# Optimization experiments

Hardware: AMD Instinct MI355X
Metric: run time of the kernel (lower is better)

The kernel has to match this reference:

```python
import jax, jax.numpy as jnp
import numpy as np

N_NODES = 50000
N_EDGES = 800000
IN_FEATS = 256
OUT_FEATS = 128


def setup_inputs() -> dict:
    key = jax.random.key(0)
    k1, k2, k3, k4 = jax.random.split(key, 4)
    feat = jax.random.normal(k1, (N_NODES, IN_FEATS), dtype=jnp.float32)
    # xavier uniform init for weight [in, out]
    limit = float(np.sqrt(6.0 / (IN_FEATS + OUT_FEATS)))
    weight = jax.random.uniform(k2, (IN_FEATS, OUT_FEATS), minval=-limit, maxval=limit, dtype=jnp.float32)
    bias = jnp.zeros((OUT_FEATS,), dtype=jnp.float32)
    src = jax.random.randint(k3, (N_EDGES,), 0, N_NODES, dtype=jnp.int32)
    dst = jax.random.randint(k4, (N_EDGES,), 0, N_NODES, dtype=jnp.int32)
    return {"feat": feat, "weight": weight, "bias": bias, "src": src, "dst": dst}


def reference(feat, weight, bias, src, dst):
    N = feat.shape[0]
    in_f, out_f = weight.shape
    # right normalization: 1 / out_degree(src node), clamped to >= 1
    deg = jax.ops.segment_sum(jnp.ones(src.shape[0], dtype=feat.dtype), src, num_segments=N)
    norm = (1.0 / jnp.maximum(deg, 1.0))[:, None]  # [N,1]
    if in_f > out_f:
        # transform first (cheaper messages), then normalize + aggregate
        h = jnp.matmul(feat, weight) * norm          # [N, out]
        rst = jax.ops.segment_sum(h[src], dst, num_segments=N)  # scatter-sum over edges
    else:
        h = feat * norm                               # [N, in]
        rst = jax.ops.segment_sum(h[src], dst, num_segments=N)
        rst = jnp.matmul(rst, weight)
    return rst + bias
```

## Files before the change

### kernel.cpp

```cpp
#include <hip/hip_runtime.h>

#define N_NODES 50000
#define N_EDGES 800000
#define IN_F 256
#define OUT_F 128

#define CHUNKS 128
#define EPC (N_EDGES / CHUNKS)
#define BINW (N_NODES / 4)
#define NWORDS (N_NODES / 4)
#define RGB 196
#define HIST_BLOCKS (2 * CHUNKS)
#define CPW (CHUNKS / 4)

#define GEMM_START HIST_BLOCKS
#define GEMMF_BLOCKS 196
#define SCAT_BLOCKS 782

typedef __attribute__((ext_vector_type(8))) short short8;
typedef __attribute__((ext_vector_type(4))) float float4_t;

__device__ __forceinline__ short f2bf(float f) {
  unsigned u = __builtin_bit_cast(unsigned, f);
  u = u + 0x7FFFu + ((u >> 16) & 1u);
  return (short)(u >> 16);
}

__device__ __forceinline__ float bflo(unsigned u) {
  return __builtin_bit_cast(float, u << 16);
}
__device__ __forceinline__ float bfhi(unsigned u) {
  return __builtin_bit_cast(float, u & 0xFFFF0000u);
}

__global__ __launch_bounds__(512) void fused1_kernel(const int* __restrict__ src,
                                                     const int* __restrict__ dst,
                                                     unsigned char* __restrict__ pdst8,
                                                     unsigned char* __restrict__ psrc8,
                                                     unsigned char* __restrict__ rank8,
                                                     const float* __restrict__ W,
                                                     const float* __restrict__ feat,
                                                     unsigned short* __restrict__ h,
                                                     int* __restrict__ cursor) {
  __shared__ uint4 smem4[4096];
  int b = blockIdx.x;
  int tid = threadIdx.x;

  if (b >= GEMM_START) {
    if (b == GEMM_START && tid == 0) *cursor = 0;
    short* wl = (short*)smem4;
#pragma unroll
    for (int i = 0; i < 64; ++i) {
      int idx = i * 512 + tid;
      int k = idx >> 7, n = idx & 127;
      int s = k >> 5, q = (k >> 3) & 3, j = k & 7;
      int tt = n >> 4, m = n & 15;
      wl[((s * 8 + tt) * 64 + q * 16 + m) * 8 + j] = f2bf(W[idx]);
    }
    __syncthreads();

    int w = tid >> 6, l = tid & 63;
    int m = l & 15, q = l >> 4;
    long base = (long)(b - GEMM_START) * 256 + w * 32;

    float4_t acc[2][8];
#pragma unroll
    for (int r = 0; r < 2; ++r)
#pragma unroll
      for (int to = 0; to < 8; ++to) acc[r][to] = (float4_t)(0.0f);

    long row0 = base + m;
    long row1 = base + 16 + m;
    long r0c = row0 < N_NODES - 1 ? row0 : N_NODES - 1;
    long r1c = row1 < N_NODES - 1 ? row1 : N_NODES - 1;
    const float* a0p = feat + (size_t)r0c * IN_F;
    const float* a1p = feat + (size_t)r1c * IN_F;
    const short8* wl8 = (const short8*)smem4;

#pragma unroll
    for (int s = 0; s < 8; ++s) {
      int k0 = s * 32 + q * 8;
      float4_t av0a = *(const float4_t*)(a0p + k0);
      float4_t av0b = *(const float4_t*)(a0p + k0 + 4);
      float4_t av1a = *(const float4_t*)(a1p + k0);
      float4_t av1b = *(const float4_t*)(a1p + k0 + 4);
      short8 fa0, fa1;
#pragma unroll
      for (int i = 0; i < 4; ++i) {
        fa0[i] = f2bf(av0a[i]);
        fa0[i + 4] = f2bf(av0b[i]);
        fa1[i] = f2bf(av1a[i]);
        fa1[i + 4] = f2bf(av1b[i]);
      }
#pragma unroll
      for (int to = 0; to < 8; ++to) {
        short8 fb = wl8[(s * 8 + to) * 64 + l];
        acc[0][to] = __builtin_amdgcn_mfma_f32_16x16x32_bf16(fa0, fb, acc[0][to], 0, 0, 0);
        acc[1][to] = __builtin_amdgcn_mfma_f32_16x16x32_bf16(fa1, fb, acc[1][to], 0, 0, 0);
      }
    }

#pragma unroll
    for (int r = 0; r < 2; ++r) {
#pragma unroll
      for (int i = 0; i < 4; ++i) {
        long row = base + r * 16 + q * 4 + i;
        if (row < N_NODES) {
          size_t ho = (size_t)row * OUT_F;
#pragma unroll
          for (int to = 0; to < 8; ++to) {
            h[ho + to * 16 + m] = (unsigned short)f2bf(acc[r][to][i]);
          }
        }
      }
    }
    return;
  }

  unsigned* bins = (unsigned*)smem4;
  int hs = b >> 7;
  int c = b & 127;
  uint4* b4 = (uint4*)bins;
  for (int j = tid; j < BINW / 4; j += 512) b4[j] = (uint4){0u, 0u, 0u, 0u};
  __syncthreads();
  const int* key = hs ? src : dst;
  int e0 = c * EPC;

  auto process = [&](int v, int eI) {
    unsigned sh = (v & 3) * 8;
    unsigned old = atomicAdd(&bins[v >> 2], 1u << sh);
    if (!hs) rank8[eI] = (unsigned char)((old >> sh) & 0xFFu);
  };

#pragma unroll 2
  for (int tile = 0; tile < 3; ++tile) {
    int i = tile * 2048 + tid;
    int k0 = key[e0 + i];
    int k1 = key[e0 + i + 512];
    int k2 = key[e0 + i + 1024];
    int k3 = key[e0 + i + 1536];
    process(k0, e0 + i);
    process(k1, e0 + i + 512);
    process(k2, e0 + i + 1024);
    process(k3, e0 + i + 1536);
  }
  {
    int i = 6144 + tid;
    if (i < EPC) process(key[e0 + i], e0 + i);
  }
  __syncthreads();
  uint4* p128 = (uint4*)((hs ? psrc8 : pdst8) + (size_t)c * N_NODES);
  const uint4* s128 = (const uint4*)bins;
  for (int j = tid; j < BINW / 4; j += 512) p128[j] = s128[j];
}

__global__ __launch_bounds__(256) void reduceoff_kernel(const unsigned char* __restrict__ pdst8,
                                                        const unsigned char* __restrict__ psrc8,
                                                        unsigned char* __restrict__ delta8,
                                                        int* __restrict__ cnt,
                                                        int* __restrict__ row_start,
                                                        int* __restrict__ cursor,
                                                        float* __restrict__ norm) {
  __shared__ unsigned tot[4][64];
  int g = blockIdx.x, side = blockIdx.y;
  int t = threadIdx.x;
  int w = t >> 6, l = t & 63;
  int wd = g * 64 + l;
  bool ok = wd < NWORDS;
  int wdc = ok ? wd : NWORDS - 1;
  const unsigned* P = (const unsigned*)(side == 0 ? pdst8 : psrc8);

  unsigned vals[CPW];
  unsigned s = 0;
#pragma unroll
  for (int i = 0; i < CPW; ++i) {
    vals[i] = P[(size_t)(w * CPW + i) * NWORDS + wdc];
    s += vals[i];
  }
  tot[w][l] = s;
  __syncthreads();

  if (side == 0) {
    unsigned base = 0;
#pragma unroll
    for (int w2 = 0; w2 < 4; ++w2)
      if (w2 < w) base += tot[w2][l];
    unsigned run = base;
    unsigned* D = (unsigned*)delta8;
    if (ok) {
#pragma unroll
      for (int i = 0; i < CPW; ++i) {
        D[(size_t)(w * CPW + i) * NWORDS + wd] = run;
        run += vals[i];
      }
    }
    if (w == 0) {
      unsigned ftot = tot[0][l] + tot[1][l] + tot[2][l] + tot[3][l];
      if (!ok) ftot = 0;
      int c0 = ftot & 255, c1 = (ftot >> 8) & 255, c2 = (ftot >> 16) & 255, c3 = ftot >> 24;
      int T = c0 + c1 + c2 + c3;
      int x = T;
#pragma unroll
      for (int off = 1; off < 64; off <<= 1) {
        int y = __shfl_up(x, off);
        if (l >= off) x += y;
      }
      int waveTotal = __shfl(x, 63);
      int sb = 0;
      if (l == 63) sb = atomicAdd(cursor, waveTotal);
      sb = __shfl(sb, 63);
      int E = sb + x - T;
      if (ok) {
        int4 cv = {c0, c1, c2, c3};
        int4 rv = {E, E + c0, E + c0 + c1, E + c0 + c1 + c2};
        ((int4*)cnt)[wd] = cv;
        ((int4*)row_start)[wd] = rv;
      }
    }
  } else {
    if (w == 0 && ok) {
      unsigned ftot = tot[0][l] + tot[1][l] + tot[2][l] + tot[3][l];
      float4 nv;
      int d0 = ftot & 255, d1 = (ftot >> 8) & 255, d2 = (ftot >> 16) & 255, d3 = (int)(ftot >> 24);
      nv.x = 1.0f / (float)(d0 > 1 ? d0 : 1);
      nv.y = 1.0f / (float)(d1 > 1 ? d1 : 1);
      nv.z = 1.0f / (float)(d2 > 1 ? d2 : 1);
      nv.w = 1.0f / (float)(d3 > 1 ? d3 : 1);
      ((float4*)norm)[wd] = nv;
    }
  }
}

__global__ __launch_bounds__(256) void scat_kernel(const int* __restrict__ src,
                                                   const int* __restrict__ dst,
                                                   const int* __restrict__ row_start,
                                                   const unsigned char* __restrict__ delta8,
                                                   const unsigned char* __restrict__ rank8,
                                                   int* __restrict__ eidx) {
  int gt = blockIdx.x * 256 + threadIdx.x;
  int e = gt * 4;
  if (e >= N_EDGES) return;
  int4 d4 = *(const int4*)(dst + e);
  int4 s4 = *(const int4*)(src + e);
  unsigned rr = *(const unsigned*)(rank8 + e);
  int dd[4] = {d4.x, d4.y, d4.z, d4.w};
  int ss[4] = {s4.x, s4.y, s4.z, s4.w};
#pragma unroll
  for (int k = 0; k < 4; ++k) {
    int c = (e + k) / EPC;
    int d = dd[k];
    int pos = row_start[d] + (int)delta8[(size_t)c * N_NODES + d] + (int)((rr >> (8 * k)) & 0xFFu);
    eidx[pos] = ss[k];
  }
}

__global__ __launch_bounds__(256) void agg_kernel(const unsigned short* __restrict__ h,
                                                  const int* __restrict__ row_start,
                                                  const int* __restrict__ cnt,
                                                  const int* __restrict__ eidx,
                                                  const float* __restrict__ norm,
                                                  const float* __restrict__ bias,
                                                  float* __restrict__ out) {
  int w = threadIdx.x >> 6, l = threadIdx.x & 63;
  int d = blockIdx.x * 4 + w;
  int rs = row_start[d], re = rs + cnt[d];
  const uint4* __restrict__ hu4 = (const uint4*)h;
  int rowsel = l >> 4;
  int cp = l & 15;
  float a0 = 0.f, a1 = 0.f, a2 = 0.f, a3 = 0.f, a4 = 0.f, a5 = 0.f, a6 = 0.f, a7 = 0.f;

  auto acc8 = [&](uint4 v, float nm) {
    a0 = fmaf(bflo(v.x), nm, a0); a1 = fmaf(bfhi(v.x), nm, a1);
    a2 = fmaf(bflo(v.y), nm, a2); a3 = fmaf(bfhi(v.y), nm, a3);
    a4 = fmaf(bflo(v.z), nm, a4); a5 = fmaf(bfhi(v.z), nm, a5);
    a6 = fmaf(bflo(v.w), nm, a6); a7 = fmaf(bfhi(v.w), nm, a7);
  };

  for (int bse = rs; bse < re; bse += 64) {
    int n = re - bse; if (n > 64) n = 64;
    int e = (l < n) ? eidx[bse + l] : 0;
    int quarter = (n + 3) >> 2;
    int j = 0;
    for (; j + 4 <= quarter; j += 4) {
      int i0 = 4 * j + rowsel;
      int s0 = __shfl(e, i0);
      int s1 = __shfl(e, i0 + 4);
      int s2 = __shfl(e, i0 + 8);
      int s3 = __shfl(e, i0 + 12);
      uint4 v0 = hu4[(size_t)s0 * 16 + cp];
      uint4 v1 = hu4[(size_t)s1 * 16 + cp];
      uint4 v2 = hu4[(size_t)s2 * 16 + cp];
      uint4 v3 = hu4[(size_t)s3 * 16 + cp];
      float nm0 = norm[s0], nm1 = norm[s1], nm2 = norm[s2], nm3 = norm[s3];
      if (i0 >= n) v0 = (uint4){0u, 0u, 0u, 0u};
      if (i0 + 4 >= n) v1 = (uint4){0u, 0u, 0u, 0u};
      if (i0 + 8 >= n) v2 = (uint4){0u, 0u, 0u, 0u};
      if (i0 + 12 >= n) v3 = (uint4){0u, 0u, 0u, 0u};
      acc8(v0, nm0);
      acc8(v1, nm1);
      acc8(v2, nm2);
      acc8(v3, nm3);
    }
    for (; j < quarter; ++j) {
      int i0 = 4 * j + rowsel;
      int s0 = __shfl(e, i0);
      uint4 v0 = hu4[(size_t)s0 * 16 + cp];
      float nm0 = norm[s0];
      if (i0 >= n) v0 = (uint4){0u, 0u, 0u, 0u};
      acc8(v0, nm0);
    }
  }
  a0 += __shfl_xor(a0, 16); a1 += __shfl_xor(a1, 16);
  a2 += __shfl_xor(a2, 16); a3 += __shfl_xor(a3, 16);
  a4 += __shfl_xor(a4, 16); a5 += __shfl_xor(a5, 16);
  a6 += __shfl_xor(a6, 16); a7 += __shfl_xor(a7, 16);
  a0 += __shfl_xor(a0, 32); a1 += __shfl_xor(a1, 32);
  a2 += __shfl_xor(a2, 32); a3 += __shfl_xor(a3, 32);
  a4 += __shfl_xor(a4, 32); a5 += __shfl_xor(a5, 32);
  a6 += __shfl_xor(a6, 32); a7 += __shfl_xor(a7, 32);
  if (rowsel == 0) {
    float4 b0 = ((const float4*)bias)[2 * cp];
    float4 b1 = ((const float4*)bias)[2 * cp + 1];
    float4 o0, o1;
    o0.x = a0 + b0.x; o0.y = a1 + b0.y; o0.z = a2 + b0.z; o0.w = a3 + b0.w;
    o1.x = a4 + b1.x; o1.y = a5 + b1.y; o1.z = a6 + b1.z; o1.w = a7 + b1.w;
    float4* op = (float4*)(out + (size_t)d * OUT_F + 8 * cp);
    op[0] = o0;
    op[1] = o1;
  }
}

extern "C" void kernel_launch(void* const* d_in, const int* in_sizes, int n_in,
                              void* d_out, int out_size, void* d_ws, size_t ws_size,
                              hipStream_t stream) {
  const float* feat = (const float*)d_in[0];
  const float* weight = (const float*)d_in[1];
  const float* bias = (const float*)d_in[2];
  const int* src = (const int*)d_in[3];
  const int* dst = (const int*)d_in[4];
  float* out = (float*)d_out;

  char* ws = (char*)d_ws;
  size_t off = 0;
  auto alloc = [&](size_t bytes) -> void* {
    void* p = ws + off;
    off += (bytes + 511) & ~(size_t)511;
    return p;
  };
  int* cursor = (int*)alloc(4);
  int* cnt = (int*)alloc(N_NODES * 4);
  int* row_start = (int*)alloc(N_NODES * 4);
  float* norm = (float*)alloc(N_NODES * 4);
  int* eidx = (int*)alloc(N_EDGES * 4);
  unsigned short* h = (unsigned short*)alloc((size_t)N_NODES * OUT_F * 2);
  unsigned char* pdst8 = (unsigned char*)alloc((size_t)CHUNKS * N_NODES);
  unsigned char* psrc8 = (unsigned char*)alloc((size_t)CHUNKS * N_NODES);
  unsigned char* delta8 = (unsigned char*)alloc((size_t)CHUNKS * N_NODES);
  unsigned char* rank8 = (unsigned char*)alloc((size_t)N_EDGES);
  (void)off; (void)ws_size; (void)in_sizes; (void)n_in; (void)out_size;

  hipLaunchKernelGGL(fused1_kernel, dim3(HIST_BLOCKS + GEMMF_BLOCKS), dim3(512), 0, stream,
                     src, dst, pdst8, psrc8, rank8, weight, feat, h, cursor);
  hipLaunchKernelGGL(reduceoff_kernel, dim3(RGB, 2), dim3(256), 0, stream,
                     pdst8, psrc8, delta8, cnt, row_start, cursor, norm);
  hipLaunchKernelGGL(scat_kernel, dim3(SCAT_BLOCKS), dim3(256), 0, stream,
                     src, dst, row_start, delta8, rank8, eidx);
  hipLaunchKernelGGL(agg_kernel, dim3(N_NODES / 4), dim3(256), 0, stream,
                     h, row_start, cnt, eidx, norm, bias, out);
}
```

Measured before the change: 170.6 us.

## Move dense GEMM blocks from histogram launch into scatter launch

```diff
diff --git a/kernel.cpp b/kernel.cpp
--- a/kernel.cpp
+++ b/kernel.cpp
@@ -13,9 +13,8 @@
 #define HIST_BLOCKS (2 * CHUNKS)
 #define CPW (CHUNKS / 4)
 
-#define GEMM_START HIST_BLOCKS
 #define GEMMF_BLOCKS 196
-#define SCAT_BLOCKS 782
+#define SCATF_BLOCKS 391
 
 typedef __attribute__((ext_vector_type(8))) short short8;
 typedef __attribute__((ext_vector_type(4))) float float4_t;
@@ -33,91 +32,16 @@
   return __builtin_bit_cast(float, u & 0xFFFF0000u);
 }
 
-__global__ __launch_bounds__(512) void fused1_kernel(const int* __restrict__ src,
-                                                     const int* __restrict__ dst,
-                                                     unsigned char* __restrict__ pdst8,
-                                                     unsigned char* __restrict__ psrc8,
-                                                     unsigned char* __restrict__ rank8,
-                                                     const float* __restrict__ W,
-                                                     const float* __restrict__ feat,
-                                                     unsigned short* __restrict__ h,
-                                                     int* __restrict__ cursor) {
-  __shared__ uint4 smem4[4096];
+__global__ __launch_bounds__(512) void hist_kernel(const int* __restrict__ src,
+                                                   const int* __restrict__ dst,
+                                                   unsigned char* __restrict__ pdst8,
+                                                   unsigned char* __restrict__ psrc8,
+                                                   unsigned char* __restrict__ rank8,
+                                                   int* __restrict__ cursor) {
+  __shared__ unsigned bins[BINW];
   int b = blockIdx.x;
   int tid = threadIdx.x;
-
-  if (b >= GEMM_START) {
-    if (b == GEMM_START && tid == 0) *cursor = 0;
-    short* wl = (short*)smem4;
-#pragma unroll
-    for (int i = 0; i < 64; ++i) {
-      int idx = i * 512 + tid;
-      int k = idx >> 7, n = idx & 127;
-      int s = k >> 5, q = (k >> 3) & 3, j = k & 7;
-      int tt = n >> 4, m = n & 15;
-      wl[((s * 8 + tt) * 64 + q * 16 + m) * 8 + j] = f2bf(W[idx]);
-    }
-    __syncthreads();
-
-    int w = tid >> 6, l = tid & 63;
-    int m = l & 15, q = l >> 4;
-    long base = (long)(b - GEMM_START) * 256 + w * 32;
-
-    float4_t acc[2][8];
-#pragma unroll
-    for (int r = 0; r < 2; ++r)
-#pragma unroll
-      for (int to = 0; to < 8; ++to) acc[r][to] = (float4_t)(0.0f);
-
-    long row0 = base + m;
-    long row1 = base + 16 + m;
-    long r0c = row0 < N_NODES - 1 ? row0 : N_NODES - 1;
-    long r1c = row1 < N_NODES - 1 ? row1 : N_NODES - 1;
-    const float* a0p = feat + (size_t)r0c * IN_F;
-    const float* a1p = feat + (size_t)r1c * IN_F;
-    const short8* wl8 = (const short8*)smem4;
-
-#pragma unroll
-    for (int s = 0; s < 8; ++s) {
-      int k0 = s * 32 + q * 8;
-      float4_t av0a = *(const float4_t*)(a0p + k0);
-      float4_t av0b = *(const float4_t*)(a0p + k0 + 4);
-      float4_t av1a = *(const float4_t*)(a1p + k0);
-      float4_t av1b = *(const float4_t*)(a1p + k0 + 4);
-      short8 fa0, fa1;
-#pragma unroll
-      for (int i = 0; i < 4; ++i) {
-        fa0[i] = f2bf(av0a[i]);
-        fa0[i + 4] = f2bf(av0b[i]);
-        fa1[i] = f2bf(av1a[i]);
-        fa1[i + 4] = f2bf(av1b[i]);
-      }
-#pragma unroll
-      for (int to = 0; to < 8; ++to) {
-        short8 fb = wl8[(s * 8 + to) * 64 + l];
-        acc[0][to] = __builtin_amdgcn_mfma_f32_16x16x32_bf16(fa0, fb, acc[0][to], 0, 0, 0);
-        acc[1][to] = __builtin_amdgcn_mfma_f32_16x16x32_bf16(fa1, fb, acc[1][to], 0, 0, 0);
-      }
-    }
-
-#pragma unroll
-    for (int r = 0; r < 2; ++r) {
-#pragma unroll
-      for (int i = 0; i < 4; ++i) {
-        long row = base + r * 16 + q * 4 + i;
-        if (row < N_NODES) {
-          size_t ho = (size_t)row * OUT_F;
-#pragma unroll
-          for (int to = 0; to < 8; ++to) {
-            h[ho + to * 16 + m] = (unsigned short)f2bf(acc[r][to][i]);
-          }
-        }
-      }
-    }
-    return;
-  }
-
-  unsigned* bins = (unsigned*)smem4;
+  if (b == 0 && tid == 0) *cursor = 0;
   int hs = b >> 7;
   int c = b & 127;
   uint4* b4 = (uint4*)bins;
@@ -231,13 +155,91 @@
   }
 }
 
-__global__ __launch_bounds__(256) void scat_kernel(const int* __restrict__ src,
-                                                   const int* __restrict__ dst,
-                                                   const int* __restrict__ row_start,
-                                                   const unsigned char* __restrict__ delta8,
-                                                   const unsigned char* __restrict__ rank8,
-                                                   int* __restrict__ eidx) {
-  int gt = blockIdx.x * 256 + threadIdx.x;
+__global__ __launch_bounds__(512) void sg_kernel(const float* __restrict__ feat,
+                                                 const float* __restrict__ W,
+                                                 unsigned short* __restrict__ h,
+                                                 const int* __restrict__ src,
+                                                 const int* __restrict__ dst,
+                                                 const int* __restrict__ row_start,
+                                                 const unsigned char* __restrict__ delta8,
+                                                 const unsigned char* __restrict__ rank8,
+                                                 int* __restrict__ eidx) {
+  __shared__ uint4 smem4[4096];
+  int b = blockIdx.x;
+  int tid = threadIdx.x;
+
+  if (b < GEMMF_BLOCKS) {
+    short* wl = (short*)smem4;
+#pragma unroll
+    for (int i = 0; i < 64; ++i) {
+      int idx = i * 512 + tid;
+      int k = idx >> 7, n = idx & 127;
+      int s = k >> 5, q = (k >> 3) & 3, j = k & 7;
+      int tt = n >> 4, m = n & 15;
+      wl[((s * 8 + tt) * 64 + q * 16 + m) * 8 + j] = f2bf(W[idx]);
+    }
+    __syncthreads();
+
+    int w = tid >> 6, l = tid & 63;
+    int m = l & 15, q = l >> 4;
+    long base = (long)b * 256 + w * 32;
+
+    float4_t acc[2][8];
+#pragma unroll
+    for (int r = 0; r < 2; ++r)
+#pragma unroll
+      for (int to = 0; to < 8; ++to) acc[r][to] = (float4_t)(0.0f);
+
+    long row0 = base + m;
+    long row1 = base + 16 + m;
+    long r0c = row0 < N_NODES - 1 ? row0 : N_NODES - 1;
+    long r1c = row1 < N_NODES - 1 ? row1 : N_NODES - 1;
+    const float* a0p = feat + (size_t)r0c * IN_F;
+    const float* a1p = feat + (size_t)r1c * IN_F;
+    const short8* wl8 = (const short8*)smem4;
+
+#pragma unroll
+    for (int s = 0; s < 8; ++s) {
+      int k0 = s * 32 + q * 8;
+      float4_t av0a = *(const float4_t*)(a0p + k0);
+      float4_t av0b = *(const float4_t*)(a0p + k0 + 4);
+      float4_t av1a = *(const float4_t*)(a1p + k0);
+      float4_t av1b = *(const float4_t*)(a1p + k0 + 4);
+      short8 fa0, fa1;
+#pragma unroll
+      for (int i = 0; i < 4; ++i) {
+        fa0[i] = f2bf(av0a[i]);
+        fa0[i + 4] = f2bf(av0b[i]);
+        fa1[i] = f2bf(av1a[i]);
+        fa1[i + 4] = f2bf(av1b[i]);
+      }
+#pragma unroll
+      for (int to = 0; to < 8; ++to) {
+        short8 fb = wl8[(s * 8 + to) * 64 + l];
+        acc[0][to] = __builtin_amdgcn_mfma_f32_16x16x32_bf16(fa0, fb, acc[0][to], 0, 0, 0);
+        acc[1][to] = __builtin_amdgcn_mfma_f32_16x16x32_bf16(fa1, fb, acc[1][to], 0, 0, 0);
+      }
+    }
+
+#pragma unroll
+    for (int r = 0; r < 2; ++r) {
+#pragma unroll
+      for (int i = 0; i < 4; ++i) {
+        long row = base + r * 16 + q * 4 + i;
+        if (row < N_NODES) {
+          size_t ho = (size_t)row * OUT_F;
+#pragma unroll
+          for (int to = 0; to < 8; ++to) {
+            h[ho + to * 16 + m] = (unsigned short)f2bf(acc[r][to][i]);
+          }
+        }
+      }
+    }
+    return;
+  }
+
+  int sb = b - GEMMF_BLOCKS;
+  int gt = sb * 512 + tid;
   int e = gt * 4;
   if (e >= N_EDGES) return;
   int4 d4 = *(const int4*)(dst + e);
@@ -359,12 +361,12 @@
   unsigned char* rank8 = (unsigned char*)alloc((size_t)N_EDGES);
   (void)off; (void)ws_size; (void)in_sizes; (void)n_in; (void)out_size;
 
-  hipLaunchKernelGGL(fused1_kernel, dim3(HIST_BLOCKS + GEMMF_BLOCKS), dim3(512), 0, stream,
-                     src, dst, pdst8, psrc8, rank8, weight, feat, h, cursor);
+  hipLaunchKernelGGL(hist_kernel, dim3(HIST_BLOCKS), dim3(512), 0, stream,
+                     src, dst, pdst8, psrc8, rank8, cursor);
   hipLaunchKernelGGL(reduceoff_kernel, dim3(RGB, 2), dim3(256), 0, stream,
                      pdst8, psrc8, delta8, cnt, row_start, cursor, norm);
-  hipLaunchKernelGGL(scat_kernel, dim3(SCAT_BLOCKS), dim3(256), 0, stream,
-                     src, dst, row_start, delta8, rank8, eidx);
+  hipLaunchKernelGGL(sg_kernel, dim3(GEMMF_BLOCKS + SCATF_BLOCKS), dim3(512), 0, stream,
+                     feat, weight, h, src, dst, row_start, delta8, rank8, eidx);
   hipLaunchKernelGGL(agg_kernel, dim3(N_NODES / 4), dim3(256), 0, stream,
                      h, row_start, cnt, eidx, norm, bias, out);
 }
```

New measurement: 171.4 us. No clear change (+0.5%).
